# Kernel optimization log

Hardware: AMD Instinct MI355X
Metric: run time of the kernel (lower is better)

## Reference

```python
import jax, jax.numpy as jnp
import numpy as np

D_MODEL = 1024
D_STATE = 16
D_CONV = 4
EXPAND = 2
D_INNER = EXPAND * D_MODEL  # 2048
DT_RANK = 64  # ceil(d_model/16)
BATCH = 2
SEQLEN = 1024
DT_MIN, DT_MAX = 0.001, 0.1


def setup_inputs() -> dict:
    key = jax.random.key(0)
    ks = jax.random.split(key, 9)
    f = jnp.float32
    hidden_states = jax.random.normal(ks[0], (BATCH, SEQLEN, D_MODEL), f)
    in_proj_w = jax.random.normal(ks[1], (2 * D_INNER, D_MODEL), f) * 0.02
    conv_w = jax.random.normal(ks[2], (D_INNER, 1, D_CONV), f) * 0.1  # depthwise: (out, in/groups=1, kw)
    conv_b = jax.random.normal(ks[3], (D_INNER,), f) * 0.01
    x_proj_w = jax.random.normal(ks[4], (DT_RANK + 2 * D_STATE, D_INNER), f) * 0.02
    std = DT_RANK ** -0.5
    dt_proj_w = jax.random.uniform(ks[5], (D_INNER, DT_RANK), f, -std, std)
    dt = jnp.exp(jax.random.uniform(ks[6], (D_INNER,), f)
                 * (np.log(DT_MAX) - np.log(DT_MIN)) + np.log(DT_MIN))
    dt = jnp.clip(dt, 1e-4, None)
    dt_proj_b = dt + jnp.log(-jnp.expm1(-dt))  # inverse softplus, as in torch init
    A_log = jnp.log(jnp.tile(jnp.arange(1, D_STATE + 1, dtype=f), (D_INNER, 1)))  # [d_inner, d_state]
    D = jnp.ones((D_INNER,), f)
    out_proj_w = jax.random.normal(ks[7], (D_MODEL, D_INNER), f) * 0.02
    return dict(hidden_states=hidden_states, in_proj_w=in_proj_w, conv_w=conv_w,
                conv_b=conv_b, x_proj_w=x_proj_w, dt_proj_w=dt_proj_w,
                dt_proj_b=dt_proj_b, A_log=A_log, D=D, out_proj_w=out_proj_w)


def reference(hidden_states, in_proj_w, conv_w, conv_b, x_proj_w,
              dt_proj_w, dt_proj_b, A_log, D, out_proj_w):
    b = hidden_states.shape[0]
    # in_proj -> split into x and gate z
    xz = hidden_states @ in_proj_w.T                      # [b, l, 2*d_inner]
    x, z = jnp.split(xz, 2, axis=-1)                      # each [b, l, d_inner]
    # causal depthwise conv over time (torch pads both sides then drops the tail)
    xc = jnp.transpose(x, (0, 2, 1))                      # [b, d_inner, l]
    xp = jnp.pad(xc, ((0, 0), (0, 0), (D_CONV - 1, 0)))
    xc = jax.lax.conv_general_dilated(
        xp, conv_w, window_strides=(1,), padding='VALID',
        feature_group_count=D_INNER,
        dimension_numbers=('NCH', 'OIH', 'NCH')) + conv_b[None, :, None]
    u = jax.nn.silu(jnp.transpose(xc, (0, 2, 1)))         # [b, l, d_inner]
    # x_proj -> dt (low-rank), B, C
    x_dbl = u @ x_proj_w.T                                # [b, l, dt_rank + 2*d_state]
    dt_low, Bm, Cm = jnp.split(x_dbl, [DT_RANK, DT_RANK + D_STATE], axis=-1)
    delta = jax.nn.softplus(dt_low @ dt_proj_w.T + dt_proj_b)  # [b, l, d_inner]
    A = -jnp.exp(A_log)                                   # [d_inner, d_state]
    # discretize
    dA = jnp.exp(jnp.einsum('bld,dn->bldn', delta, A))    # [b, l, d_inner, d_state]
    dBu = (delta * u)[..., None] * Bm[:, :, None, :]      # [b, l, d_inner, d_state]
    # sequential selective scan over l
    xs = (jnp.moveaxis(dA, 1, 0), jnp.moveaxis(dBu, 1, 0), jnp.moveaxis(Cm, 1, 0))
    h0 = jnp.zeros((b, D_INNER, D_STATE), hidden_states.dtype)

    def step(h, inp):
        dA_t, dBu_t, C_t = inp
        h = dA_t * h + dBu_t                              # [b, d_inner, d_state]
        y_t = jnp.einsum('bdn,bn->bd', h, C_t)
        return h, y_t

    _, ys = jax.lax.scan(step, h0, xs)                    # ys: [l, b, d_inner]
    y = jnp.moveaxis(ys, 0, 1) + u * D                    # skip connection
    y = y * jax.nn.silu(z)                                # gate
    return y @ out_proj_w.T                               # [b, l, d_model]
```

## Files before the change

kernel.cpp:

```cpp
#include <hip/hip_runtime.h>
#include <hip/hip_bf16.h>
#include <math.h>

typedef __attribute__((ext_vector_type(8))) short short8;
typedef __attribute__((ext_vector_type(4))) float floatx4;
typedef unsigned short u16;
typedef unsigned int u32;

__device__ __forceinline__ float b2f(u16 v) {
    union { u32 i; float f; } x; x.i = ((u32)v) << 16; return x.f;
}
__device__ __forceinline__ u16 f2b(float f) {
    union { u32 i; float f; } x; x.f = f;
    u32 r = x.i + 0x7FFFu + ((x.i >> 16) & 1u);
    return (u16)(r >> 16);
}

#define BM 128
#define BN 128
#define BKg 64
#define NCHUNK 16
#define CT 64

__global__ void convert_all(const float* __restrict__ s0, u16* __restrict__ d0,
                            const float* __restrict__ s1, u16* __restrict__ d1,
                            const float* __restrict__ s2, u16* __restrict__ d2,
                            const float* __restrict__ s3, u16* __restrict__ d3,
                            const float* __restrict__ s4, u16* __restrict__ d4)
{
    int i = blockIdx.x * 256 + threadIdx.x;
    const float* src; u16* dst;
    if (i < 524288)            { src = s0; dst = d0; }
    else if (i < 1572864)      { src = s1; dst = d1; i -= 524288; }
    else if (i < 1622016)      { src = s2; dst = d2; i -= 1572864; }
    else if (i < 1654784)      { src = s3; dst = d3; i -= 1622016; }
    else if (i < 2179072)      { src = s4; dst = d4; i -= 1654784; }
    else return;
    float4 v = ((const float4*)src)[i];
    ushort4 o;
    o.x = f2b(v.x); o.y = f2b(v.y); o.z = f2b(v.z); o.w = f2b(v.w);
    ((ushort4*)dst)[i] = o;
}

template<int EPI>
__global__ __launch_bounds__(256, 2)
void gemm_nt(const u16* __restrict__ A, const u16* __restrict__ B,
             void* __restrict__ Cout, const float* __restrict__ bias,
             int M, int N, int K_per_split, int lda, int ldb, int ldc)
{
    __shared__ __align__(16) short As[BM][BKg + 8];
    __shared__ __align__(16) short Bs[BN][BKg + 8];

    const int tid  = threadIdx.x;
    const int wave = tid >> 6;
    const int lane = tid & 63;
    const int m0 = blockIdx.x * BM;
    const int n0 = blockIdx.y * BN;
    const int k_begin = blockIdx.z * K_per_split;

    const int wm = (wave & 1) * 64;
    const int wn = (wave >> 1) * 64;

    floatx4 acc[4][4];
#pragma unroll
    for (int i = 0; i < 4; i++)
#pragma unroll
        for (int j = 0; j < 4; j++) acc[i][j] = (floatx4)(0.f);

    const int srow = tid >> 1;
    const int scol = (tid & 1) * 32;

    for (int k0 = 0; k0 < K_per_split; k0 += BKg) {
        const int kg = k_begin + k0;
        const u16* ag = A + (size_t)(m0 + srow) * lda + kg + scol;
        uint4 a0 = ((const uint4*)ag)[0];
        uint4 a1 = ((const uint4*)ag)[1];
        uint4 a2 = ((const uint4*)ag)[2];
        uint4 a3 = ((const uint4*)ag)[3];
        uint4 b0 = make_uint4(0,0,0,0), b1 = make_uint4(0,0,0,0);
        uint4 b2 = make_uint4(0,0,0,0), b3 = make_uint4(0,0,0,0);
        if (n0 + srow < N) {
            const u16* bg = B + (size_t)(n0 + srow) * ldb + kg + scol;
            b0 = ((const uint4*)bg)[0];
            b1 = ((const uint4*)bg)[1];
            b2 = ((const uint4*)bg)[2];
            b3 = ((const uint4*)bg)[3];
        }
        __syncthreads();
        *(uint4*)&As[srow][scol]      = a0;
        *(uint4*)&As[srow][scol + 8]  = a1;
        *(uint4*)&As[srow][scol + 16] = a2;
        *(uint4*)&As[srow][scol + 24] = a3;
        *(uint4*)&Bs[srow][scol]      = b0;
        *(uint4*)&Bs[srow][scol + 8]  = b1;
        *(uint4*)&Bs[srow][scol + 16] = b2;
        *(uint4*)&Bs[srow][scol + 24] = b3;
        __syncthreads();
#pragma unroll
        for (int kk = 0; kk < 2; kk++) {
            const int ko = kk * 32 + (lane >> 4) * 8;
            short8 af[4], bfr[4];
#pragma unroll
            for (int i = 0; i < 4; i++)
                af[i] = *(const short8*)&As[wm + i * 16 + (lane & 15)][ko];
#pragma unroll
            for (int j = 0; j < 4; j++)
                bfr[j] = *(const short8*)&Bs[wn + j * 16 + (lane & 15)][ko];
#pragma unroll
            for (int i = 0; i < 4; i++)
#pragma unroll
                for (int j = 0; j < 4; j++)
                    acc[i][j] = __builtin_amdgcn_mfma_f32_16x16x32_bf16(
                        af[i], bfr[j], acc[i][j], 0, 0, 0);
        }
    }

    const int cn0 = n0 + wn + (lane & 15);
    const int cm0 = m0 + wm + ((lane >> 4) << 2);
    const size_t zoff = (size_t)blockIdx.z * M * ldc;
#pragma unroll
    for (int i = 0; i < 4; i++) {
#pragma unroll
        for (int j = 0; j < 4; j++) {
            const int n = cn0 + j * 16;
            if (n < N) {
#pragma unroll
                for (int r = 0; r < 4; r++) {
                    const int m = cm0 + i * 16 + r;
                    float v = acc[i][j][r];
                    const size_t off = (size_t)m * ldc + n;
                    if constexpr (EPI == 1) {
                        ((u16*)Cout)[off] = f2b(v);
                    } else if constexpr (EPI == 3) {
                        v += bias[n];
                        float sp = (v > 15.f) ? v : log1pf(__expf(v));
                        ((float*)Cout)[off] = sp;
                    } else {
                        ((float*)Cout)[zoff + off] = v;
                    }
                }
            }
        }
    }
}

__global__ void reduce_xdbl(const float* __restrict__ part, float* __restrict__ of,
                            u16* __restrict__ ob)
{
    const int i = blockIdx.x * 256 + threadIdx.x;
    if (i >= 49152) return;
    const size_t MN4 = 49152;
    float4 s = ((const float4*)part)[i];
#pragma unroll
    for (int z = 1; z < 16; z++) {
        const float4 p = ((const float4*)part)[z * MN4 + i];
        s.x += p.x; s.y += p.y; s.z += p.z; s.w += p.w;
    }
    ((float4*)of)[i] = s;
    ushort4 o;
    o.x = f2b(s.x); o.y = f2b(s.y); o.z = f2b(s.z); o.w = f2b(s.w);
    ((ushort4*)ob)[i] = o;
}

__global__ void reduce_out(const float* __restrict__ part, float* __restrict__ out)
{
    const int i = blockIdx.x * 256 + threadIdx.x;
    const size_t MN4 = 524288;
    float4 s = ((const float4*)part)[i];
#pragma unroll
    for (int z = 1; z < 4; z++) {
        const float4 p = ((const float4*)part)[z * MN4 + i];
        s.x += p.x; s.y += p.y; s.z += p.z; s.w += p.w;
    }
    ((float4*)out)[i] = s;
}

__global__ void conv_silu_kernel(const u16* __restrict__ xz, const float* __restrict__ cw,
                                 const float* __restrict__ cb, u16* __restrict__ u)
{
    const int idx = blockIdx.x * 256 + threadIdx.x;
    const int d = idx & 2047;
    const int row = idx >> 11;
    const int l = row & 1023;
    float acc = cb[d];
#pragma unroll
    for (int j = 0; j < 4; j++) {
        const int lj = l - 3 + j;
        if (lj >= 0)
            acc += cw[d * 4 + j] * b2f(xz[(size_t)(row - 3 + j) * 4096 + d]);
    }
    const float s = acc / (1.f + __expf(-acc));
    u[(size_t)row * 2048 + d] = f2b(s);
}

__global__ __launch_bounds__(256)
void scan_pass1(const float* __restrict__ delta, const u16* __restrict__ u,
                const float* __restrict__ xdbl, const float* __restrict__ A_log,
                float* __restrict__ aP, float* __restrict__ hpart)
{
    __shared__ float dS[CT * 128];
    __shared__ u16   uS[CT * 128];
    __shared__ float BS[CT * 16];

    const int tid  = threadIdx.x;
    const int half = tid & 1;
    const int dloc = tid >> 1;
    const int d0 = blockIdx.x * 128;
    const int d = d0 + dloc;
    const int b = blockIdx.y >> 4;
    const int chunk = blockIdx.y & 15;
    const int bd = b * 2048 + d;
    const size_t row0 = (size_t)b * 1024 + chunk * CT;

    for (int i = tid; i < CT * 128 / 4; i += 256) {
        const int e = i * 4;
        const int t = e >> 7, c = e & 127;
        *(float4*)&dS[e] = *(const float4*)&delta[(row0 + t) * 2048 + d0 + c];
    }
    for (int i = tid; i < CT * 128 / 8; i += 256) {
        const int e = i * 8;
        const int t = e >> 7, c = e & 127;
        *(uint4*)&uS[e] = *(const uint4*)&u[(row0 + t) * 2048 + d0 + c];
    }
    for (int i = tid; i < CT * 16; i += 256) {
        const int t = i >> 4, n = i & 15;
        BS[i] = xdbl[(row0 + t) * 96 + 64 + n];
    }

    float A_dn[8], h[8], ap[8];
#pragma unroll
    for (int j = 0; j < 8; j++) {
        A_dn[j] = -__expf(A_log[d * 16 + half * 8 + j]);
        h[j] = 0.f; ap[j] = 1.f;
    }
    __syncthreads();

#pragma unroll 4
    for (int t = 0; t < CT; t++) {
        const float dl = dS[t * 128 + dloc];
        const float uu = b2f(uS[t * 128 + dloc]);
        const float dlu = dl * uu;
        const float4 B0 = *(const float4*)&BS[t * 16 + half * 8];
        const float4 B1 = *(const float4*)&BS[t * 16 + half * 8 + 4];
        const float Bv[8] = {B0.x, B0.y, B0.z, B0.w, B1.x, B1.y, B1.z, B1.w};
#pragma unroll
        for (int j = 0; j < 8; j++) {
            const float dA = __expf(dl * A_dn[j]);
            h[j] = dA * h[j] + dlu * Bv[j];
            ap[j] *= dA;
        }
    }

    const size_t o = ((size_t)(bd * 16 + chunk) * 16) + half * 8;
    *(float4*)&aP[o]     = make_float4(ap[0], ap[1], ap[2], ap[3]);
    *(float4*)&aP[o + 4] = make_float4(ap[4], ap[5], ap[6], ap[7]);
    *(float4*)&hpart[o]     = make_float4(h[0], h[1], h[2], h[3]);
    *(float4*)&hpart[o + 4] = make_float4(h[4], h[5], h[6], h[7]);
}

__global__ void scan_combine(const float* __restrict__ aP, float* __restrict__ hp)
{
    const int idx = blockIdx.x * 256 + threadIdx.x;
    const int n = idx & 15;
    const int bd = idx >> 4;
    float h = 0.f;
    for (int c = 0; c < NCHUNK; c++) {
        const size_t o = ((size_t)(bd * 16 + c) * 16) + n;
        const float a = aP[o];
        const float p = hp[o];
        hp[o] = h;
        h = a * h + p;
    }
}

__global__ __launch_bounds__(256)
void scan_pass2(const float* __restrict__ delta, const u16* __restrict__ u,
                const float* __restrict__ xdbl, const u16* __restrict__ xz,
                const float* __restrict__ A_log, const float* __restrict__ Dv,
                const float* __restrict__ hinit, u16* __restrict__ ybuf)
{
    __shared__ float dS[CT * 128];
    __shared__ u16   uS[CT * 128];
    __shared__ u16   zS[CT * 128];
    __shared__ float BS[CT * 16];
    __shared__ float CS[CT * 16];

    const int tid  = threadIdx.x;
    const int half = tid & 1;
    const int dloc = tid >> 1;
    const int d0 = blockIdx.x * 128;
    const int d = d0 + dloc;
    const int b = blockIdx.y >> 4;
    const int chunk = blockIdx.y & 15;
    const int bd = b * 2048 + d;
    const size_t row0 = (size_t)b * 1024 + chunk * CT;

    for (int i = tid; i < CT * 128 / 4; i += 256) {
        const int e = i * 4;
        const int t = e >> 7, c = e & 127;
        *(float4*)&dS[e] = *(const float4*)&delta[(row0 + t) * 2048 + d0 + c];
    }
    for (int i = tid; i < CT * 128 / 8; i += 256) {
        const int e = i * 8;
        const int t = e >> 7, c = e & 127;
        *(uint4*)&uS[e] = *(const uint4*)&u[(row0 + t) * 2048 + d0 + c];
        *(uint4*)&zS[e] = *(const uint4*)&xz[(row0 + t) * 4096 + 2048 + d0 + c];
    }
    for (int i = tid; i < CT * 16; i += 256) {
        const int t = i >> 4, n = i & 15;
        BS[i] = xdbl[(row0 + t) * 96 + 64 + n];
        CS[i] = xdbl[(row0 + t) * 96 + 80 + n];
    }

    const size_t o = ((size_t)(bd * 16 + chunk) * 16) + half * 8;
    const float4 h0 = *(const float4*)&hinit[o];
    const float4 h1 = *(const float4*)&hinit[o + 4];
    float h[8] = {h0.x, h0.y, h0.z, h0.w, h1.x, h1.y, h1.z, h1.w};
    float A_dn[8];
#pragma unroll
    for (int j = 0; j < 8; j++)
        A_dn[j] = -__expf(A_log[d * 16 + half * 8 + j]);
    const float Dd = Dv[d];
    __syncthreads();

#pragma unroll 4
    for (int t = 0; t < CT; t++) {
        const float dl = dS[t * 128 + dloc];
        const float uu = b2f(uS[t * 128 + dloc]);
        const float dlu = dl * uu;
        const float4 B0 = *(const float4*)&BS[t * 16 + half * 8];
        const float4 B1 = *(const float4*)&BS[t * 16 + half * 8 + 4];
        const float4 C0 = *(const float4*)&CS[t * 16 + half * 8];
        const float4 C1 = *(const float4*)&CS[t * 16 + half * 8 + 4];
        const float Bv[8] = {B0.x, B0.y, B0.z, B0.w, B1.x, B1.y, B1.z, B1.w};
        const float Cv[8] = {C0.x, C0.y, C0.z, C0.w, C1.x, C1.y, C1.z, C1.w};
        float p = 0.f;
#pragma unroll
        for (int j = 0; j < 8; j++) {
            const float dA = __expf(dl * A_dn[j]);
            h[j] = dA * h[j] + dlu * Bv[j];
            p += h[j] * Cv[j];
        }
        p += __shfl_xor(p, 1);
        if (half == 0) {
            const float z = b2f(zS[t * 128 + dloc]);
            const float gt = z / (1.f + __expf(-z));
            ybuf[(row0 + t) * 2048 + d] = f2b((p + uu * Dd) * gt);
        }
    }
}

extern "C" void kernel_launch(void* const* d_in, const int* in_sizes, int n_in,
                              void* d_out, int out_size, void* d_ws, size_t ws_size,
                              hipStream_t stream)
{
    const float* hid    = (const float*)d_in[0];
    const float* w_in   = (const float*)d_in[1];
    const float* conv_w = (const float*)d_in[2];
    const float* conv_b = (const float*)d_in[3];
    const float* w_x    = (const float*)d_in[4];
    const float* w_dt   = (const float*)d_in[5];
    const float* b_dt   = (const float*)d_in[6];
    const float* A_log  = (const float*)d_in[7];
    const float* Dvec   = (const float*)d_in[8];
    const float* w_out  = (const float*)d_in[9];
    float* out = (float*)d_out;

    const size_t MB = 1048576;
    char* ws = (char*)d_ws;
    u16*   xz     = (u16*)(ws + 0);
    u16*   ubuf   = (u16*)(ws + 16 * MB);
    float* part3  = (float*)(ws + 24 * MB);
    float* delta  = (float*)(ws + 24 * MB);
    float* part6  = (float*)(ws + 0);
    float* xdblf  = (float*)(ws + 40 * MB);
    u16*   xdblb  = (u16*)(ws + 40 * MB + 786432);
    u16*   w_x_b  = (u16*)(ws + 41 * MB + 131072);
    u16*   w_dt_b = (u16*)(ws + 41 * MB + 524288);
    u16*   hid_b  = (u16*)(ws + 42 * MB);
    float* hpart  = (float*)(ws + 42 * MB);
    u16*   w_in_b = (u16*)(ws + 46 * MB);
    float* aP     = (float*)(ws + 50 * MB);
    u16*   ybuf   = (u16*)(ws + 46 * MB);
    u16*   w_out_b= (u16*)(ws + 54 * MB);

    convert_all<<<8512, 256, 0, stream>>>(hid, hid_b, w_in, w_in_b, w_x, w_x_b,
                                          w_dt, w_dt_b, w_out, w_out_b);

    gemm_nt<1><<<dim3(16, 32, 1), 256, 0, stream>>>(hid_b, w_in_b, xz, nullptr,
                                                    2048, 4096, 1024, 1024, 1024, 4096);
    conv_silu_kernel<<<16384, 256, 0, stream>>>(xz, conv_w, conv_b, ubuf);
    gemm_nt<5><<<dim3(16, 1, 16), 256, 0, stream>>>(ubuf, w_x_b, part3, nullptr,
                                                    2048, 96, 128, 2048, 2048, 96);
    reduce_xdbl<<<192, 256, 0, stream>>>(part3, xdblf, xdblb);
    gemm_nt<3><<<dim3(16, 16, 1), 256, 0, stream>>>(xdblb, w_dt_b, delta, b_dt,
                                                    2048, 2048, 64, 96, 64, 2048);
    scan_pass1<<<dim3(16, 32), 256, 0, stream>>>(delta, ubuf, xdblf, A_log, aP, hpart);
    scan_combine<<<256, 256, 0, stream>>>(aP, hpart);
    scan_pass2<<<dim3(16, 32), 256, 0, stream>>>(delta, ubuf, xdblf, xz, A_log, Dvec,
                                                 hpart, ybuf);
    gemm_nt<5><<<dim3(16, 8, 4), 256, 0, stream>>>(ybuf, w_out_b, part6, nullptr,
                                                   2048, 1024, 512, 2048, 2048, 1024);
    reduce_out<<<2048, 256, 0, stream>>>(part6, out);
}
```

Baseline: 264.9 us.

## Load GEMM tiles directly into LDS and store delta as bf16

The GEMM tile loads now use global_load_lds to move data straight from global memory into shared memory, skipping the register staging step. The LDS padding is dropped and the occupancy hint rises to 4 blocks per CU. Separately, the dt-projection epilogue writes softplus(delta) as bf16 rather than fp32, so both scan passes read half the bytes for delta. Without padding, the MFMA fragment reads from LDS may hit bank conflicts, and bf16 delta reduces precision inside the exponent of the scan.

```diff
diff --git a/kernel.cpp b/kernel.cpp
--- a/kernel.cpp
+++ b/kernel.cpp
@@ -14,6 +14,11 @@
     union { u32 i; float f; } x; x.f = f;
     u32 r = x.i + 0x7FFFu + ((x.i >> 16) & 1u);
     return (u16)(r >> 16);
+}
+
+__device__ __forceinline__ void gload_lds16(const u16* g, short* l) {
+    __builtin_amdgcn_global_load_lds((const __attribute__((address_space(1))) void*)g,
+                                     (__attribute__((address_space(3))) void*)l, 16, 0, 0);
 }
 
 #define BM 128
@@ -43,13 +48,13 @@
 }
 
 template<int EPI>
-__global__ __launch_bounds__(256, 2)
+__global__ __launch_bounds__(256, 4)
 void gemm_nt(const u16* __restrict__ A, const u16* __restrict__ B,
              void* __restrict__ Cout, const float* __restrict__ bias,
              int M, int N, int K_per_split, int lda, int ldb, int ldc)
 {
-    __shared__ __align__(16) short As[BM][BKg + 8];
-    __shared__ __align__(16) short Bs[BN][BKg + 8];
+    __shared__ __align__(16) short As[BM][BKg];
+    __shared__ __align__(16) short Bs[BN][BKg];
 
     const int tid  = threadIdx.x;
     const int wave = tid >> 6;
@@ -67,34 +72,23 @@
 #pragma unroll
         for (int j = 0; j < 4; j++) acc[i][j] = (floatx4)(0.f);
 
-    const int srow = tid >> 1;
-    const int scol = (tid & 1) * 32;
+    const int srow = wave * 32 + (lane >> 3);
+    const int scol = (lane & 7) * 8;
 
     for (int k0 = 0; k0 < K_per_split; k0 += BKg) {
         const int kg = k_begin + k0;
-        const u16* ag = A + (size_t)(m0 + srow) * lda + kg + scol;
-        uint4 a0 = ((const uint4*)ag)[0];
-        uint4 a1 = ((const uint4*)ag)[1];
-        uint4 a2 = ((const uint4*)ag)[2];
-        uint4 a3 = ((const uint4*)ag)[3];
-        uint4 b0 = make_uint4(0,0,0,0), b1 = make_uint4(0,0,0,0);
-        uint4 b2 = make_uint4(0,0,0,0), b3 = make_uint4(0,0,0,0);
-        if (n0 + srow < N) {
-            const u16* bg = B + (size_t)(n0 + srow) * ldb + kg + scol;
-            b0 = ((const uint4*)bg)[0];
-            b1 = ((const uint4*)bg)[1];
-            b2 = ((const uint4*)bg)[2];
-            b3 = ((const uint4*)bg)[3];
-        }
         __syncthreads();
-        *(uint4*)&As[srow][scol]      = a0;
-        *(uint4*)&As[srow][scol + 8]  = a1;
-        *(uint4*)&As[srow][scol + 16] = a2;
-        *(uint4*)&As[srow][scol + 24] = a3;
-        *(uint4*)&Bs[srow][scol]      = b0;
-        *(uint4*)&Bs[srow][scol + 8]  = b1;
-        *(uint4*)&Bs[srow][scol + 16] = b2;
-        *(uint4*)&Bs[srow][scol + 24] = b3;
+#pragma unroll
+        for (int j = 0; j < 4; j++) {
+            const int r = srow + j * 8;
+            gload_lds16(A + (size_t)(m0 + r) * lda + kg + scol, &As[r][scol]);
+        }
+#pragma unroll
+        for (int j = 0; j < 4; j++) {
+            const int r = srow + j * 8;
+            if (n0 + r < N)
+                gload_lds16(B + (size_t)(n0 + r) * ldb + kg + scol, &Bs[r][scol]);
+        }
         __syncthreads();
 #pragma unroll
         for (int kk = 0; kk < 2; kk++) {
@@ -131,10 +125,10 @@
                     const size_t off = (size_t)m * ldc + n;
                     if constexpr (EPI == 1) {
                         ((u16*)Cout)[off] = f2b(v);
-                    } else if constexpr (EPI == 3) {
+                    } else if constexpr (EPI == 6) {
                         v += bias[n];
                         float sp = (v > 15.f) ? v : log1pf(__expf(v));
-                        ((float*)Cout)[off] = sp;
+                        ((u16*)Cout)[off] = f2b(sp);
                     } else {
                         ((float*)Cout)[zoff + off] = v;
                     }
@@ -194,11 +188,11 @@
 }
 
 __global__ __launch_bounds__(256)
-void scan_pass1(const float* __restrict__ delta, const u16* __restrict__ u,
+void scan_pass1(const u16* __restrict__ delta, const u16* __restrict__ u,
                 const float* __restrict__ xdbl, const float* __restrict__ A_log,
                 float* __restrict__ aP, float* __restrict__ hpart)
 {
-    __shared__ float dS[CT * 128];
+    __shared__ u16   dS[CT * 128];
     __shared__ u16   uS[CT * 128];
     __shared__ float BS[CT * 16];
 
@@ -212,14 +206,10 @@
     const int bd = b * 2048 + d;
     const size_t row0 = (size_t)b * 1024 + chunk * CT;
 
-    for (int i = tid; i < CT * 128 / 4; i += 256) {
-        const int e = i * 4;
-        const int t = e >> 7, c = e & 127;
-        *(float4*)&dS[e] = *(const float4*)&delta[(row0 + t) * 2048 + d0 + c];
-    }
     for (int i = tid; i < CT * 128 / 8; i += 256) {
         const int e = i * 8;
         const int t = e >> 7, c = e & 127;
+        *(uint4*)&dS[e] = *(const uint4*)&delta[(row0 + t) * 2048 + d0 + c];
         *(uint4*)&uS[e] = *(const uint4*)&u[(row0 + t) * 2048 + d0 + c];
     }
     for (int i = tid; i < CT * 16; i += 256) {
@@ -237,7 +227,7 @@
 
 #pragma unroll 4
     for (int t = 0; t < CT; t++) {
-        const float dl = dS[t * 128 + dloc];
+        const float dl = b2f(dS[t * 128 + dloc]);
         const float uu = b2f(uS[t * 128 + dloc]);
         const float dlu = dl * uu;
         const float4 B0 = *(const float4*)&BS[t * 16 + half * 8];
@@ -274,12 +264,12 @@
 }
 
 __global__ __launch_bounds__(256)
-void scan_pass2(const float* __restrict__ delta, const u16* __restrict__ u,
+void scan_pass2(const u16* __restrict__ delta, const u16* __restrict__ u,
                 const float* __restrict__ xdbl, const u16* __restrict__ xz,
                 const float* __restrict__ A_log, const float* __restrict__ Dv,
                 const float* __restrict__ hinit, u16* __restrict__ ybuf)
 {
-    __shared__ float dS[CT * 128];
+    __shared__ u16   dS[CT * 128];
     __shared__ u16   uS[CT * 128];
     __shared__ u16   zS[CT * 128];
     __shared__ float BS[CT * 16];
@@ -295,14 +285,10 @@
     const int bd = b * 2048 + d;
     const size_t row0 = (size_t)b * 1024 + chunk * CT;
 
-    for (int i = tid; i < CT * 128 / 4; i += 256) {
-        const int e = i * 4;
-        const int t = e >> 7, c = e & 127;
-        *(float4*)&dS[e] = *(const float4*)&delta[(row0 + t) * 2048 + d0 + c];
-    }
     for (int i = tid; i < CT * 128 / 8; i += 256) {
         const int e = i * 8;
         const int t = e >> 7, c = e & 127;
+        *(uint4*)&dS[e] = *(const uint4*)&delta[(row0 + t) * 2048 + d0 + c];
         *(uint4*)&uS[e] = *(const uint4*)&u[(row0 + t) * 2048 + d0 + c];
         *(uint4*)&zS[e] = *(const uint4*)&xz[(row0 + t) * 4096 + 2048 + d0 + c];
     }
@@ -325,7 +311,7 @@
 
 #pragma unroll 4
     for (int t = 0; t < CT; t++) {
-        const float dl = dS[t * 128 + dloc];
+        const float dl = b2f(dS[t * 128 + dloc]);
         const float uu = b2f(uS[t * 128 + dloc]);
         const float dlu = dl * uu;
         const float4 B0 = *(const float4*)&BS[t * 16 + half * 8];
@@ -371,7 +357,7 @@
     u16*   xz     = (u16*)(ws + 0);
     u16*   ubuf   = (u16*)(ws + 16 * MB);
     float* part3  = (float*)(ws + 24 * MB);
-    float* delta  = (float*)(ws + 24 * MB);
+    u16*   delta  = (u16*)(ws + 24 * MB);
     float* part6  = (float*)(ws + 0);
     float* xdblf  = (float*)(ws + 40 * MB);
     u16*   xdblb  = (u16*)(ws + 40 * MB + 786432);
@@ -393,7 +379,7 @@
     gemm_nt<5><<<dim3(16, 1, 16), 256, 0, stream>>>(ubuf, w_x_b, part3, nullptr,
                                                     2048, 96, 128, 2048, 2048, 96);
     reduce_xdbl<<<192, 256, 0, stream>>>(part3, xdblf, xdblb);
-    gemm_nt<3><<<dim3(16, 16, 1), 256, 0, stream>>>(xdblb, w_dt_b, delta, b_dt,
+    gemm_nt<6><<<dim3(16, 16, 1), 256, 0, stream>>>(xdblb, w_dt_b, delta, b_dt,
                                                     2048, 2048, 64, 96, 64, 2048);
     scan_pass1<<<dim3(16, 32), 256, 0, stream>>>(delta, ubuf, xdblf, A_log, aP, hpart);
     scan_combine<<<256, 256, 0, stream>>>(aP, hpart);
```

Result: slower. 294.5 us (+11.2%).
